# Performance work log

Measured on AMD Instinct MI355X. Metric: run time of the kernel, lower is better.

The kernel has to match this reference:

```python
import jax, jax.numpy as jnp
import numpy as np

B, S, D, H = 2, 2048, 1024, 16
HD = D // H  # 64


def setup_inputs() -> dict:
    key = jax.random.key(0)
    ks = jax.random.split(key, 10)
    sc = 1.0 / np.sqrt(D)
    return {
        "decoder_hs": jax.random.normal(ks[0], (B, S, D), jnp.float32),
        "encoder_hs": jax.random.normal(ks[1], (B, S, D), jnp.float32),
        "Wq": jax.random.normal(ks[2], (D, D), jnp.float32) * sc,
        "bq": jax.random.normal(ks[3], (D,), jnp.float32) * 0.02,
        "Wk": jax.random.normal(ks[4], (D, D), jnp.float32) * sc,
        "bk": jax.random.normal(ks[5], (D,), jnp.float32) * 0.02,
        "Wv": jax.random.normal(ks[6], (D, D), jnp.float32) * sc,
        "bv": jax.random.normal(ks[7], (D,), jnp.float32) * 0.02,
        "Wp": jax.random.normal(ks[8], (D, D), jnp.float32) * sc,
        "bp": jax.random.normal(ks[9], (D,), jnp.float32) * 0.02,
    }


def reference(decoder_hs, encoder_hs, Wq, bq, Wk, bk, Wv, bv, Wp, bp):
    b, s, d = decoder_hs.shape
    # torch nn.Linear: y = x @ W.T + b, W is [out, in]
    q = decoder_hs @ Wq.T + bq
    k = encoder_hs @ Wk.T + bk
    v = encoder_hs @ Wv.T + bv
    # head split: [b, s, d] -> [b, h, s, hd]
    q = q.reshape(b, s, H, HD).transpose(0, 2, 1, 3)
    k = k.reshape(b, s, H, HD).transpose(0, 2, 1, 3)
    v = v.reshape(b, s, H, HD).transpose(0, 2, 1, 3)
    scale = 1.0 / np.sqrt(HD).astype(np.float32)
    att = jnp.einsum('bhqd,bhkd->bhqk', q, k) * scale
    att = jax.nn.softmax(att, axis=-1)
    y = jnp.einsum('bhqk,bhkd->bhqd', att, v)
    y = y.transpose(0, 2, 1, 3).reshape(b, s, d)
    return y @ Wp.T + bp
```

## Files before the change

kernel.cpp:

```cpp
#include <hip/hip_runtime.h>
#include <hip/hip_bf16.h>
#include <cstdint>
#include <cstddef>

#define BB 2
#define SS 2048
#define DD 1024
#define HH 16
#define HD 64

typedef __attribute__((ext_vector_type(8))) short bf16x8;
typedef __attribute__((ext_vector_type(4))) float f32x4;
typedef __attribute__((ext_vector_type(16))) float f32x16;

#define GLL(g, l) __builtin_amdgcn_global_load_lds( \
    (const __attribute__((address_space(1))) void*)(g), \
    (__attribute__((address_space(3))) void*)(l), 16, 0, 0)

__device__ __forceinline__ short f2bf_fast(float f) {
    uint32_t u = __float_as_uint(f);
    u += 0x7FFF + ((u >> 16) & 1);
    return (short)(u >> 16);
}
__device__ __forceinline__ uint32_t pack_bf2(float a, float b) {
    uint32_t ua = __float_as_uint(a), ub = __float_as_uint(b);
    ua += 0x7FFF + ((ua >> 16) & 1);
    ub += 0x7FFF + ((ub >> 16) & 1);
    return (ua >> 16) | (ub & 0xFFFF0000u);
}
__device__ __forceinline__ uint32_t cvtpk_bf2(float a, float b) {
    uint32_t r;
    asm("v_cvt_pk_bf16_f32 %0, %1, %2" : "=v"(r) : "v"(a), "v"(b));
    return r;
}
__device__ __forceinline__ void pl32swap(uint32_t& a, uint32_t& b) {
    asm("v_permlane32_swap_b32 %0, %1" : "+v"(a), "+v"(b));
}
__device__ __forceinline__ bf16x8 cvt8(const float* __restrict__ p) {
    float4 a = *(const float4*)p;
    float4 b = *(const float4*)(p + 4);
    union { uint32_t d[4]; bf16x8 v; } r;
    r.d[0] = pack_bf2(a.x, a.y);
    r.d[1] = pack_bf2(a.z, a.w);
    r.d[2] = pack_bf2(b.x, b.y);
    r.d[3] = pack_bf2(b.z, b.w);
    return r.v;
}

__global__ __launch_bounds__(256) void cvt6_kernel(
    const float* __restrict__ s0, const float* __restrict__ s1,
    const float* __restrict__ s2, const float* __restrict__ s3,
    const float* __restrict__ s4, const float* __restrict__ s5,
    short* __restrict__ d0, short* __restrict__ d1, short* __restrict__ d2,
    short* __restrict__ d3, short* __restrict__ d4, short* __restrict__ d5)
{
    const int id = blockIdx.x * 256 + threadIdx.x;
    const float* s; short* d; size_t off;
    if (id < 1048576) {
        int e = id >> 19;
        off = (size_t)(id & 524287) * 8;
        s = e ? s1 : s0;  d = e ? d1 : d0;
    } else {
        int j = id - 1048576;
        int w = j >> 17;
        off = (size_t)(j & 131071) * 8;
        s = (w == 0) ? s2 : (w == 1) ? s3 : (w == 2) ? s4 : s5;
        d = (w == 0) ? d2 : (w == 1) ? d3 : (w == 2) ? d4 : d5;
    }
    bf16x8 r = cvt8(s + off);
    *(uint4*)(d + off) = *(uint4*)&r;
}

template<int BF>
__global__ __launch_bounds__(256, 3) void qkv_gemm_kernel(
    const void* __restrict__ dec, const void* __restrict__ enc,
    const void* __restrict__ Wq, const void* __restrict__ Wk,
    const void* __restrict__ Wv,
    const float* __restrict__ bq, const float* __restrict__ bk,
    const float* __restrict__ bv,
    short* __restrict__ Qo, short* __restrict__ Ko, short* __restrict__ Vo)
{
    __shared__ short As[128 * 64];
    __shared__ short Bs[128 * 64];

    const int z = blockIdx.z;
    const void* Xv = (z == 0) ? dec : enc;
    const void* Wp_ = (z == 0) ? Wq : (z == 1) ? Wk : Wv;
    const float* bias = (z == 0) ? bq : (z == 1) ? bk : bv;
    short* Yo = (z == 0) ? Qo : (z == 1) ? Ko : Vo;
    const float qs = (z == 0) ? (0.125f * 1.44269504088896f) : 1.0f;

    const int t = threadIdx.x;
    const int lane = t & 63, wv = t >> 6;
    const int lr = lane & 15, quad = lane >> 4;
    const int e7 = lr & 7;
    const int wm = wv >> 1, wn = wv & 1;
    const int m0 = blockIdx.y * 128;
    const int n0 = blockIdx.x * 128;
    const int K = DD;

    f32x4 acc[4][4];
    #pragma unroll
    for (int i = 0; i < 4; i++)
        #pragma unroll
        for (int j = 0; j < 4; j++) acc[i][j] = (f32x4){0.f, 0.f, 0.f, 0.f};

    for (int kb = 0; kb < K; kb += 64) {
        __syncthreads();
        if (BF) {
            const short* Xb = (const short*)Xv;
            const short* Wb = (const short*)Wp_;
            #pragma unroll
            for (int c = 0; c < 4; c++) {
                int r0 = wv * 32 + c * 8;
                int r = r0 + (lane >> 3);
                int sc = ((lane & 7) ^ (r & 7)) * 8;
                GLL(Xb + (size_t)(m0 + r) * K + kb + sc, &As[r0 * 64]);
                GLL(Wb + (size_t)(n0 + r) * K + kb + sc, &Bs[r0 * 64]);
            }
        } else {
            const float* Xf = (const float*)Xv;
            const float* Wf = (const float*)Wp_;
            #pragma unroll
            for (int c = 0; c < 4; c++) {
                int id = t + c * 256;
                int r = id >> 3, lc = id & 7;
                int pc = (lc ^ (r & 7)) * 8;
                *(bf16x8*)&As[r * 64 + pc] = cvt8(Xf + (size_t)(m0 + r) * K + kb + lc * 8);
                *(bf16x8*)&Bs[r * 64 + pc] = cvt8(Wf + (size_t)(n0 + r) * K + kb + lc * 8);
            }
        }
        __syncthreads();

        bf16x8 af[4][2], bfr[4][2];
        #pragma unroll
        for (int kk = 0; kk < 2; kk++) {
            int pc = ((kk * 4 + quad) ^ e7) * 8;
            #pragma unroll
            for (int mi = 0; mi < 4; mi++)
                af[mi][kk] = *(const bf16x8*)&As[(wm * 64 + mi * 16 + lr) * 64 + pc];
            #pragma unroll
            for (int ni = 0; ni < 4; ni++)
                bfr[ni][kk] = *(const bf16x8*)&Bs[(wn * 64 + ni * 16 + lr) * 64 + pc];
        }
        #pragma unroll
        for (int kk = 0; kk < 2; kk++)
            #pragma unroll
            for (int mi = 0; mi < 4; mi++)
                #pragma unroll
                for (int ni = 0; ni < 4; ni++)
                    acc[mi][ni] = __builtin_amdgcn_mfma_f32_16x16x32_bf16(
                        af[mi][kk], bfr[ni][kk], acc[mi][ni], 0, 0, 0);
    }

    if (z < 2) {
        #pragma unroll
        for (int ni = 0; ni < 4; ni++) {
            int col = n0 + wn * 64 + ni * 16 + lr;
            int h = col >> 6, hd = col & 63;
            float bvv = bias[col];
            #pragma unroll
            for (int mi = 0; mi < 4; mi++) {
                #pragma unroll
                for (int r2 = 0; r2 < 4; r2++) {
                    int row = m0 + wm * 64 + mi * 16 + quad * 4 + r2;
                    int b = row >> 11, s = row & 2047;
                    float v = (acc[mi][ni][r2] + bvv) * qs;
                    size_t off = ((size_t)(b * HH + h) * SS + s) * HD + hd;
                    Yo[off] = f2bf_fast(v);
                }
            }
        }
    } else {
        #pragma unroll
        for (int ni = 0; ni < 4; ni++) {
            int col = n0 + wn * 64 + ni * 16 + lr;
            int h = col >> 6, hd = col & 63;
            float bvv = bias[col];
            #pragma unroll
            for (int mi = 0; mi < 4; mi++) {
                int s0 = m0 + wm * 64 + mi * 16 + quad * 4;
                int b = s0 >> 11, s = s0 & 2047;
                union { uint32_t d[2]; } u;
                u.d[0] = pack_bf2(acc[mi][ni][0] + bvv, acc[mi][ni][1] + bvv);
                u.d[1] = pack_bf2(acc[mi][ni][2] + bvv, acc[mi][ni][3] + bvv);
                size_t off = ((size_t)(b * HH + h) * HD + hd) * SS + s;
                *(uint2*)(Yo + off) = *(uint2*)&u;
            }
        }
    }
}

template<int WBF>
__global__ __launch_bounds__(256, 2) void proj_gemm_kernel(
    const short* __restrict__ X,
    const void* __restrict__ W, const float* __restrict__ bias,
    float* __restrict__ Y)
{
    __shared__ short As[64 * 32];
    __shared__ short Bs[128 * 32];

    const int t = threadIdx.x;
    const int lane = t & 63, wv = t >> 6;
    const int lr = lane & 15, quad = lane >> 4;
    const int wm = wv >> 1, wn = wv & 1;
    const int m0 = blockIdx.y * 64;
    const int n0 = blockIdx.x * 128;
    const int K = DD, N = DD;

    f32x4 acc[2][4];
    #pragma unroll
    for (int i = 0; i < 2; i++)
        #pragma unroll
        for (int j = 0; j < 4; j++) acc[i][j] = (f32x4){0.f, 0.f, 0.f, 0.f};

    for (int kb = 0; kb < K; kb += 32) {
        __syncthreads();
        {
            int r0 = wv * 16;
            int r = r0 + (lane >> 2), ch = (lane & 3) * 8;
            GLL(X + (size_t)(m0 + r) * K + kb + ch, &As[r0 * 32]);
        }
        if (WBF) {
            const short* Wb = (const short*)W;
            #pragma unroll
            for (int c = 0; c < 2; c++) {
                int r0 = wv * 32 + c * 16;
                int r = r0 + (lane >> 2), ch = (lane & 3) * 8;
                GLL(Wb + (size_t)(n0 + r) * K + kb + ch, &Bs[r0 * 32]);
            }
        } else {
            const float* Wf = (const float*)W;
            #pragma unroll
            for (int c = 0; c < 2; c++) {
                int id = t + c * 256;
                int r = id >> 2, c8 = (id & 3) * 8;
                *(bf16x8*)&Bs[r * 32 + c8] = cvt8(Wf + (size_t)(n0 + r) * K + kb + c8);
            }
        }
        __syncthreads();

        bf16x8 af[2], bfr[4];
        #pragma unroll
        for (int mi = 0; mi < 2; mi++)
            af[mi] = *(const bf16x8*)&As[(wm * 32 + mi * 16 + lr) * 32 + quad * 8];
        #pragma unroll
        for (int ni = 0; ni < 4; ni++)
            bfr[ni] = *(const bf16x8*)&Bs[(wn * 64 + ni * 16 + lr) * 32 + quad * 8];
        #pragma unroll
        for (int mi = 0; mi < 2; mi++)
            #pragma unroll
            for (int ni = 0; ni < 4; ni++)
                acc[mi][ni] = __builtin_amdgcn_mfma_f32_16x16x32_bf16(
                    af[mi], bfr[ni], acc[mi][ni], 0, 0, 0);
    }

    #pragma unroll
    for (int ni = 0; ni < 4; ni++) {
        int col = n0 + wn * 64 + ni * 16 + lr;
        float bvv = bias[col];
        #pragma unroll
        for (int mi = 0; mi < 2; mi++) {
            #pragma unroll
            for (int r2 = 0; r2 < 4; r2++) {
                int row = m0 + wm * 32 + mi * 16 + quad * 4 + r2;
                Y[(size_t)row * N + col] = acc[mi][ni][r2] + bvv;
            }
        }
    }
}

__global__ __launch_bounds__(256, 2) void attn_kernel(
    const short* __restrict__ Q,
    const short* __restrict__ Kgl,
    const short* __restrict__ Vt_g,
    short* __restrict__ Y)
{
    __shared__ short Ks[2][128][64];
    __shared__ short Vt[2][64][128];

    const int t = threadIdx.x;
    const int lane = t & 63, w = t >> 6;
    const int lq = lane & 31, hf = lane >> 5;
    const int gl = (lq & 7) ^ ((lq >> 3) & 3);

    const int bid = blockIdx.x;
    const int slot = bid >> 3;
    const int bh = ((slot >> 4) << 3) + (bid & 7);
    const int qt = slot & 15;
    const int b = bh >> 4, h = bh & 15;

    const int q = qt * 128 + w * 32 + lq;
    const short* Qp = Q + ((size_t)bh * SS + q) * HD;
    bf16x8 qf[4];
    #pragma unroll
    for (int j = 0; j < 4; j++)
        qf[j] = *(const bf16x8*)(Qp + j * 16 + hf * 8);

    f32x16 o[2];
    #pragma unroll
    for (int i = 0; i < 16; i++) { o[0][i] = 0.f; o[1][i] = 0.f; }
    f32x4 vsum = (f32x4){0.f, 0.f, 0.f, 0.f};

    const short* Kb = Kgl + (size_t)bh * SS * HD;
    const short* Vb = Vt_g + (size_t)bh * HD * SS;

    auto stage = [&](int kt1, int nb) {
        #pragma unroll
        for (int c = 0; c < 4; c++) {
            int r0 = w * 32 + c * 8;
            int r  = r0 + (lane >> 3);
            int g  = (r & 7) ^ ((r >> 3) & 3);
            int sc = ((lane & 7) ^ g) * 8;
            GLL(Kb + (size_t)(kt1 * 128 + r) * 64 + sc, &Ks[nb][r0][0]);
        }
        #pragma unroll
        for (int c = 0; c < 4; c++) {
            int h0 = w * 16 + c * 4;
            int hd = h0 + (lane >> 4);
            int g  = (hd & 7) ^ ((hd >> 3) & 3);
            int s16 = (lane & 15) ^ g;
            GLL(Vb + (size_t)hd * SS + kt1 * 128 + s16 * 8, &Vt[nb][h0][0]);
        }
    };

    stage(0, 0);
    __syncthreads();

    int cur = 0;
    for (int kt = 0; kt < SS / 128; kt++) {
        if (kt + 1 < SS / 128) stage(kt + 1, cur ^ 1);

        bf16x8 pb[4][2];
        #pragma unroll
        for (int s = 0; s < 4; s++) {
            const short* krow = &Ks[cur][s * 32 + lq][0];
            f32x16 sc = (f32x16){0.f,0.f,0.f,0.f,0.f,0.f,0.f,0.f,
                                 0.f,0.f,0.f,0.f,0.f,0.f,0.f,0.f};
            __builtin_amdgcn_s_setprio(1);
            #pragma unroll
            for (int j = 0; j < 4; j++) {
                bf16x8 kf = *(const bf16x8*)&krow[((j * 2 + hf) ^ gl) * 8];
                sc = __builtin_amdgcn_mfma_f32_32x32x16_bf16(kf, qf[j], sc, 0, 0, 0);
            }
            __builtin_amdgcn_s_setprio(0);

            float ev[16];
            #pragma unroll
            for (int i = 0; i < 16; i++) ev[i] = __builtin_amdgcn_exp2f(sc[i]);
            #pragma unroll
            for (int r = 0; r < 4; r++)
                vsum += (f32x4){ev[4*r], ev[4*r+1], ev[4*r+2], ev[4*r+3]};
            uint32_t dw[8];
            #pragma unroll
            for (int i = 0; i < 8; i++) dw[i] = cvtpk_bf2(ev[2*i], ev[2*i+1]);
            pl32swap(dw[0], dw[2]); pl32swap(dw[1], dw[3]);
            pl32swap(dw[4], dw[6]); pl32swap(dw[5], dw[7]);
            union { uint32_t u[4]; bf16x8 v; } f0, f1;
            f0.u[0] = dw[0]; f0.u[1] = dw[1]; f0.u[2] = dw[2]; f0.u[3] = dw[3];
            f1.u[0] = dw[4]; f1.u[1] = dw[5]; f1.u[2] = dw[6]; f1.u[3] = dw[7];
            pb[s][0] = f0.v; pb[s][1] = f1.v;
        }

        __builtin_amdgcn_s_setprio(1);
        #pragma unroll
        for (int ds = 0; ds < 2; ds++) {
            const short* vrow = &Vt[cur][ds * 32 + lq][0];
            #pragma unroll
            for (int s = 0; s < 4; s++)
                #pragma unroll
                for (int c = 0; c < 2; c++) {
                    bf16x8 va = *(const bf16x8*)&vrow[((s * 4 + c * 2 + hf) ^ gl) * 8];
                    o[ds] = __builtin_amdgcn_mfma_f32_32x32x16_bf16(
                        va, pb[s][c], o[ds], 0, 0, 0);
                }
        }
        __builtin_amdgcn_s_setprio(0);

        __syncthreads();
        cur ^= 1;
    }

    float lsum = (vsum[0] + vsum[1]) + (vsum[2] + vsum[3]);
    lsum += __shfl_xor(lsum, 32, 64);
    float inv = 1.0f / lsum;

    short* Yp = Y + ((size_t)b * SS + q) * DD + h * 64 + hf * 4;
    #pragma unroll
    for (int ds = 0; ds < 2; ds++)
        #pragma unroll
        for (int rr = 0; rr < 4; rr++) {
            union { uint32_t d[2]; } u;
            u.d[0] = pack_bf2(o[ds][rr*4+0] * inv, o[ds][rr*4+1] * inv);
            u.d[1] = pack_bf2(o[ds][rr*4+2] * inv, o[ds][rr*4+3] * inv);
            *(uint2*)(Yp + ds * 32 + rr * 8) = *(uint2*)&u;
        }
}

extern "C" void kernel_launch(void* const* d_in, const int* in_sizes, int n_in,
                              void* d_out, int out_size, void* d_ws, size_t ws_size,
                              hipStream_t stream) {
    const float* dec = (const float*)d_in[0];
    const float* enc = (const float*)d_in[1];
    const float* Wq  = (const float*)d_in[2];
    const float* bq  = (const float*)d_in[3];
    const float* Wk  = (const float*)d_in[4];
    const float* bk  = (const float*)d_in[5];
    const float* Wv  = (const float*)d_in[6];
    const float* bv  = (const float*)d_in[7];
    const float* Wp  = (const float*)d_in[8];
    const float* bp  = (const float*)d_in[9];

    const size_t per = (size_t)BB * HH * SS * HD;
    const size_t wsz = (size_t)DD * DD;
    short* ws = (short*)d_ws;
    short* Qb  = ws;
    short* Kb  = ws + per;
    short* Vtb = ws + 2 * per;
    short* Yb  = ws + 3 * per;

    dim3 qkv_grid(DD / 128, (BB * SS) / 128, 3);
    dim3 proj_grid(DD / 128, (BB * SS) / 64);
    const int attn_blocks = BB * HH * (SS / 128);
    const int cvt_blocks = (2 * 524288 + 4 * 131072) / 256;

    const size_t need = (6 * per + 4 * wsz) * sizeof(short);
    if (ws_size >= need) {
        short* decb = ws + 4 * per;
        short* encb = ws + 5 * per;
        short* Wqb  = ws + 6 * per;
        short* Wkb  = Wqb + wsz;
        short* Wvb  = Wqb + 2 * wsz;
        short* Wpb  = Wqb + 3 * wsz;
        cvt6_kernel<<<cvt_blocks, 256, 0, stream>>>(
            dec, enc, Wq, Wk, Wv, Wp, decb, encb, Wqb, Wkb, Wvb, Wpb);
        qkv_gemm_kernel<1><<<qkv_grid, 256, 0, stream>>>(
            decb, encb, Wqb, Wkb, Wvb, bq, bk, bv, Qb, Kb, Vtb);
        attn_kernel<<<attn_blocks, 256, 0, stream>>>(Qb, Kb, Vtb, Yb);
        proj_gemm_kernel<1><<<proj_grid, 256, 0, stream>>>(Yb, Wpb, bp, (float*)d_out);
    } else {
        qkv_gemm_kernel<0><<<qkv_grid, 256, 0, stream>>>(
            dec, enc, Wq, Wk, Wv, bq, bk, bv, Qb, Kb, Vtb);
        attn_kernel<<<attn_blocks, 256, 0, stream>>>(Qb, Kb, Vtb, Yb);
        proj_gemm_kernel<0><<<proj_grid, 256, 0, stream>>>(Yb, Wp, bp, (float*)d_out);
    }
}
```

Before: 195.5 us.

## Double K-tile in projection GEMM with XOR swizzle; interleave QK MFMA chains in attention

The projection GEMM now stages 64-wide K slices instead of 32, which halves the number of barrier-separated iterations. It also adds an XOR swizzle to the LDS layout so the wider rows are read without bank conflicts. In the attention kernel, the four independent QK^T accumulation chains are computed interleaved before any exponentiation, so consecutive MFMAs do not depend on each other. The cost is doubled LDS use in the GEMM and more live accumulator registers in attention, which could lower occupancy.

```diff
diff --git a/kernel.cpp b/kernel.cpp
--- a/kernel.cpp
+++ b/kernel.cpp
@@ -197,12 +197,13 @@
     const void* __restrict__ W, const float* __restrict__ bias,
     float* __restrict__ Y)
 {
-    __shared__ short As[64 * 32];
-    __shared__ short Bs[128 * 32];
+    __shared__ short As[64 * 64];
+    __shared__ short Bs[128 * 64];
 
     const int t = threadIdx.x;
     const int lane = t & 63, wv = t >> 6;
     const int lr = lane & 15, quad = lane >> 4;
+    const int e7 = lr & 7;
     const int wm = wv >> 1, wn = wv & 1;
     const int m0 = blockIdx.y * 64;
     const int n0 = blockIdx.x * 128;
@@ -214,45 +215,57 @@
         #pragma unroll
         for (int j = 0; j < 4; j++) acc[i][j] = (f32x4){0.f, 0.f, 0.f, 0.f};
 
-    for (int kb = 0; kb < K; kb += 32) {
+    for (int kb = 0; kb < K; kb += 64) {
         __syncthreads();
         {
-            int r0 = wv * 16;
-            int r = r0 + (lane >> 2), ch = (lane & 3) * 8;
-            GLL(X + (size_t)(m0 + r) * K + kb + ch, &As[r0 * 32]);
+            #pragma unroll
+            for (int c = 0; c < 2; c++) {
+                int r0 = wv * 16 + c * 8;
+                int r = r0 + (lane >> 3);
+                int sc = ((lane & 7) ^ (r & 7)) * 8;
+                GLL(X + (size_t)(m0 + r) * K + kb + sc, &As[r0 * 64]);
+            }
         }
         if (WBF) {
             const short* Wb = (const short*)W;
             #pragma unroll
-            for (int c = 0; c < 2; c++) {
-                int r0 = wv * 32 + c * 16;
-                int r = r0 + (lane >> 2), ch = (lane & 3) * 8;
-                GLL(Wb + (size_t)(n0 + r) * K + kb + ch, &Bs[r0 * 32]);
+            for (int c = 0; c < 4; c++) {
+                int r0 = wv * 32 + c * 8;
+                int r = r0 + (lane >> 3);
+                int sc = ((lane & 7) ^ (r & 7)) * 8;
+                GLL(Wb + (size_t)(n0 + r) * K + kb + sc, &Bs[r0 * 64]);
             }
         } else {
             const float* Wf = (const float*)W;
             #pragma unroll
-            for (int c = 0; c < 2; c++) {
+            for (int c = 0; c < 4; c++) {
                 int id = t + c * 256;
-                int r = id >> 2, c8 = (id & 3) * 8;
-                *(bf16x8*)&Bs[r * 32 + c8] = cvt8(Wf + (size_t)(n0 + r) * K + kb + c8);
+                int r = id >> 3, lc = id & 7;
+                int pc = (lc ^ (r & 7)) * 8;
+                *(bf16x8*)&Bs[r * 64 + pc] = cvt8(Wf + (size_t)(n0 + r) * K + kb + lc * 8);
             }
         }
         __syncthreads();
 
-        bf16x8 af[2], bfr[4];
-        #pragma unroll
-        for (int mi = 0; mi < 2; mi++)
-            af[mi] = *(const bf16x8*)&As[(wm * 32 + mi * 16 + lr) * 32 + quad * 8];
-        #pragma unroll
-        for (int ni = 0; ni < 4; ni++)
-            bfr[ni] = *(const bf16x8*)&Bs[(wn * 64 + ni * 16 + lr) * 32 + quad * 8];
-        #pragma unroll
-        for (int mi = 0; mi < 2; mi++)
+        bf16x8 af[2][2], bfr[4][2];
+        #pragma unroll
+        for (int kk = 0; kk < 2; kk++) {
+            int pc = ((kk * 4 + quad) ^ e7) * 8;
+            #pragma unroll
+            for (int mi = 0; mi < 2; mi++)
+                af[mi][kk] = *(const bf16x8*)&As[(wm * 32 + mi * 16 + lr) * 64 + pc];
             #pragma unroll
             for (int ni = 0; ni < 4; ni++)
-                acc[mi][ni] = __builtin_amdgcn_mfma_f32_16x16x32_bf16(
-                    af[mi], bfr[ni], acc[mi][ni], 0, 0, 0);
+                bfr[ni][kk] = *(const bf16x8*)&Bs[(wn * 64 + ni * 16 + lr) * 64 + pc];
+        }
+        #pragma unroll
+        for (int kk = 0; kk < 2; kk++)
+            #pragma unroll
+            for (int mi = 0; mi < 2; mi++)
+                #pragma unroll
+                for (int ni = 0; ni < 4; ni++)
+                    acc[mi][ni] = __builtin_amdgcn_mfma_f32_16x16x32_bf16(
+                        af[mi][kk], bfr[ni][kk], acc[mi][ni], 0, 0, 0);
     }
 
     #pragma unroll
@@ -331,23 +344,29 @@
     for (int kt = 0; kt < SS / 128; kt++) {
         if (kt + 1 < SS / 128) stage(kt + 1, cur ^ 1);
 
+        f32x16 sc[4];
+        #pragma unroll
+        for (int s = 0; s < 4; s++)
+            #pragma unroll
+            for (int i = 0; i < 16; i++) sc[s][i] = 0.f;
+        __builtin_amdgcn_s_setprio(1);
+        #pragma unroll
+        for (int j = 0; j < 4; j++)
+            #pragma unroll
+            for (int s = 0; s < 4; s++) {
+                const short* krow = &Ks[cur][s * 32 + lq][0];
+                bf16x8 kf = *(const bf16x8*)&krow[((j * 2 + hf) ^ gl) * 8];
+                sc[s] = __builtin_amdgcn_mfma_f32_32x32x16_bf16(
+                    kf, qf[j], sc[s], 0, 0, 0);
+            }
+        __builtin_amdgcn_s_setprio(0);
+
         bf16x8 pb[4][2];
         #pragma unroll
         for (int s = 0; s < 4; s++) {
-            const short* krow = &Ks[cur][s * 32 + lq][0];
-            f32x16 sc = (f32x16){0.f,0.f,0.f,0.f,0.f,0.f,0.f,0.f,
-                                 0.f,0.f,0.f,0.f,0.f,0.f,0.f,0.f};
-            __builtin_amdgcn_s_setprio(1);
-            #pragma unroll
-            for (int j = 0; j < 4; j++) {
-                bf16x8 kf = *(const bf16x8*)&krow[((j * 2 + hf) ^ gl) * 8];
-                sc = __builtin_amdgcn_mfma_f32_32x32x16_bf16(kf, qf[j], sc, 0, 0, 0);
-            }
-            __builtin_amdgcn_s_setprio(0);
-
             float ev[16];
             #pragma unroll
-            for (int i = 0; i < 16; i++) ev[i] = __builtin_amdgcn_exp2f(sc[i]);
+            for (int i = 0; i < 16; i++) ev[i] = __builtin_amdgcn_exp2f(sc[s][i]);
             #pragma unroll
             for (int r = 0; r < 4; r++)
                 vsum += (f32x4){ev[4*r], ev[4*r+1], ev[4*r+2], ev[4*r+3]};
```

After: 199.1 us. About the same (+1.8%).

## Give each wave private K/V LDS tiles and drop block-wide barriers

Applied to the files above, without the earlier changes.

Each of the four waves now stages its own copy of the K and V^T tiles, 32 keys per step, into a private LDS region. Block-wide __syncthreads are replaced with per-wave waitcnt and sched_barrier. The aim is to remove cross-wave barrier stalls so waves can drift independently. In exchange every wave loads the full K/V stream itself, quadrupling global/L2 traffic per block. The shorter key tile also doubles loop iterations and leaves less MFMA work per iteration to hide load latency.

```diff
diff --git a/kernel.cpp b/kernel.cpp
--- a/kernel.cpp
+++ b/kernel.cpp
@@ -276,13 +276,13 @@
     const short* __restrict__ Vt_g,
     short* __restrict__ Y)
 {
-    __shared__ short Ks[2][128][64];
-    __shared__ short Vt[2][64][128];
+    __shared__ short smem[32768];
 
     const int t = threadIdx.x;
     const int lane = t & 63, w = t >> 6;
     const int lq = lane & 31, hf = lane >> 5;
     const int gl = (lq & 7) ^ ((lq >> 3) & 3);
+    const int vl = lq & 3;
 
     const int bid = blockIdx.x;
     const int slot = bid >> 3;
@@ -305,79 +305,76 @@
     const short* Kb = Kgl + (size_t)bh * SS * HD;
     const short* Vb = Vt_g + (size_t)bh * HD * SS;
 
+    short* wbase = smem + w * 8192;
+
     auto stage = [&](int kt1, int nb) {
+        short* Kd = wbase + nb * 2048;
+        short* Vd = wbase + 4096 + nb * 2048;
         #pragma unroll
         for (int c = 0; c < 4; c++) {
-            int r0 = w * 32 + c * 8;
-            int r  = r0 + (lane >> 3);
-            int g  = (r & 7) ^ ((r >> 3) & 3);
+            int r = c * 8 + (lane >> 3);
+            int g = (r & 7) ^ ((r >> 3) & 3);
             int sc = ((lane & 7) ^ g) * 8;
-            GLL(Kb + (size_t)(kt1 * 128 + r) * 64 + sc, &Ks[nb][r0][0]);
+            GLL(Kb + (size_t)(kt1 * 32 + r) * HD + sc, Kd + c * 8 * 64);
         }
         #pragma unroll
         for (int c = 0; c < 4; c++) {
-            int h0 = w * 16 + c * 4;
-            int hd = h0 + (lane >> 4);
-            int g  = (hd & 7) ^ ((hd >> 3) & 3);
-            int s16 = (lane & 15) ^ g;
-            GLL(Vb + (size_t)hd * SS + kt1 * 128 + s16 * 8, &Vt[nb][h0][0]);
+            int hd = c * 16 + (lane >> 2);
+            int sc = ((lane & 3) ^ (hd & 3)) * 8;
+            GLL(Vb + (size_t)hd * SS + kt1 * 32 + sc, Vd + c * 16 * 32);
         }
     };
 
     stage(0, 0);
-    __syncthreads();
+    asm volatile("s_waitcnt vmcnt(0)" ::: "memory");
+    __builtin_amdgcn_sched_barrier(0);
 
     int cur = 0;
-    for (int kt = 0; kt < SS / 128; kt++) {
-        if (kt + 1 < SS / 128) stage(kt + 1, cur ^ 1);
-
-        bf16x8 pb[4][2];
-        #pragma unroll
-        for (int s = 0; s < 4; s++) {
-            const short* krow = &Ks[cur][s * 32 + lq][0];
-            f32x16 sc = (f32x16){0.f,0.f,0.f,0.f,0.f,0.f,0.f,0.f,
-                                 0.f,0.f,0.f,0.f,0.f,0.f,0.f,0.f};
-            __builtin_amdgcn_s_setprio(1);
-            #pragma unroll
-            for (int j = 0; j < 4; j++) {
-                bf16x8 kf = *(const bf16x8*)&krow[((j * 2 + hf) ^ gl) * 8];
-                sc = __builtin_amdgcn_mfma_f32_32x32x16_bf16(kf, qf[j], sc, 0, 0, 0);
-            }
-            __builtin_amdgcn_s_setprio(0);
-
-            float ev[16];
-            #pragma unroll
-            for (int i = 0; i < 16; i++) ev[i] = __builtin_amdgcn_exp2f(sc[i]);
-            #pragma unroll
-            for (int r = 0; r < 4; r++)
-                vsum += (f32x4){ev[4*r], ev[4*r+1], ev[4*r+2], ev[4*r+3]};
-            uint32_t dw[8];
-            #pragma unroll
-            for (int i = 0; i < 8; i++) dw[i] = cvtpk_bf2(ev[2*i], ev[2*i+1]);
-            pl32swap(dw[0], dw[2]); pl32swap(dw[1], dw[3]);
-            pl32swap(dw[4], dw[6]); pl32swap(dw[5], dw[7]);
-            union { uint32_t u[4]; bf16x8 v; } f0, f1;
-            f0.u[0] = dw[0]; f0.u[1] = dw[1]; f0.u[2] = dw[2]; f0.u[3] = dw[3];
-            f1.u[0] = dw[4]; f1.u[1] = dw[5]; f1.u[2] = dw[6]; f1.u[3] = dw[7];
-            pb[s][0] = f0.v; pb[s][1] = f1.v;
-        }
-
+    for (int kt = 0; kt < SS / 32; kt++) {
+        if (kt + 1 < SS / 32) stage(kt + 1, cur ^ 1);
+
+        const short* Kc = wbase + cur * 2048;
+        const short* Vc = wbase + 4096 + cur * 2048;
+
+        f32x16 sc16 = (f32x16){0.f,0.f,0.f,0.f,0.f,0.f,0.f,0.f,
+                               0.f,0.f,0.f,0.f,0.f,0.f,0.f,0.f};
         __builtin_amdgcn_s_setprio(1);
         #pragma unroll
+        for (int j = 0; j < 4; j++) {
+            bf16x8 kf = *(const bf16x8*)&Kc[lq * 64 + ((j * 2 + hf) ^ gl) * 8];
+            sc16 = __builtin_amdgcn_mfma_f32_32x32x16_bf16(kf, qf[j], sc16, 0, 0, 0);
+        }
+        __builtin_amdgcn_s_setprio(0);
+
+        float ev[16];
+        #pragma unroll
+        for (int i = 0; i < 16; i++) ev[i] = __builtin_amdgcn_exp2f(sc16[i]);
+        #pragma unroll
+        for (int r = 0; r < 4; r++)
+            vsum += (f32x4){ev[4*r], ev[4*r+1], ev[4*r+2], ev[4*r+3]};
+        uint32_t dw[8];
+        #pragma unroll
+        for (int i = 0; i < 8; i++) dw[i] = cvtpk_bf2(ev[2*i], ev[2*i+1]);
+        pl32swap(dw[0], dw[2]); pl32swap(dw[1], dw[3]);
+        pl32swap(dw[4], dw[6]); pl32swap(dw[5], dw[7]);
+        union { uint32_t u[4]; bf16x8 v; } f0, f1;
+        f0.u[0] = dw[0]; f0.u[1] = dw[1]; f0.u[2] = dw[2]; f0.u[3] = dw[3];
+        f1.u[0] = dw[4]; f1.u[1] = dw[5]; f1.u[2] = dw[6]; f1.u[3] = dw[7];
+        bf16x8 pb0 = f0.v, pb1 = f1.v;
+
+        __builtin_amdgcn_s_setprio(1);
+        #pragma unroll
         for (int ds = 0; ds < 2; ds++) {
-            const short* vrow = &Vt[cur][ds * 32 + lq][0];
-            #pragma unroll
-            for (int s = 0; s < 4; s++)
-                #pragma unroll
-                for (int c = 0; c < 2; c++) {
-                    bf16x8 va = *(const bf16x8*)&vrow[((s * 4 + c * 2 + hf) ^ gl) * 8];
-                    o[ds] = __builtin_amdgcn_mfma_f32_32x32x16_bf16(
-                        va, pb[s][c], o[ds], 0, 0, 0);
-                }
+            const short* vrow = &Vc[(ds * 32 + lq) * 32];
+            bf16x8 va0 = *(const bf16x8*)&vrow[((0 + hf) ^ vl) * 8];
+            o[ds] = __builtin_amdgcn_mfma_f32_32x32x16_bf16(va0, pb0, o[ds], 0, 0, 0);
+            bf16x8 va1 = *(const bf16x8*)&vrow[((2 + hf) ^ vl) * 8];
+            o[ds] = __builtin_amdgcn_mfma_f32_32x32x16_bf16(va1, pb1, o[ds], 0, 0, 0);
         }
         __builtin_amdgcn_s_setprio(0);
 
-        __syncthreads();
+        asm volatile("s_waitcnt vmcnt(0) lgkmcnt(0)" ::: "memory");
+        __builtin_amdgcn_sched_barrier(0);
         cur ^= 1;
     }
 
```

After: 207.1 us. +6.0%, slower.

## Software-pipeline attention: overlap PV of previous tile with softmax of current

Applied to the files above, without the earlier changes.

Restructures the attention loop so QK^T for tile kt is issued in one batch, then the PV matmuls for tile kt-1 are interleaved with the exp/convert softmax work of tile kt using sched_group_barrier hints. V is triple-buffered in LDS so the previous tile's V stays resident while the next one streams in. The aim is to hide transcendental and VALU latency behind MFMA work. In exchange it uses more LDS and registers (two P buffers, four score accumulators), which may pressure occupancy at 2 blocks per CU.

```diff
diff --git a/kernel.cpp b/kernel.cpp
--- a/kernel.cpp
+++ b/kernel.cpp
@@ -277,7 +277,7 @@
     short* __restrict__ Y)
 {
     __shared__ short Ks[2][128][64];
-    __shared__ short Vt[2][64][128];
+    __shared__ short Vt[3][64][128];
 
     const int t = threadIdx.x;
     const int lane = t & 63, w = t >> 6;
@@ -305,14 +305,16 @@
     const short* Kb = Kgl + (size_t)bh * SS * HD;
     const short* Vb = Vt_g + (size_t)bh * HD * SS;
 
-    auto stage = [&](int kt1, int nb) {
+    auto stage = [&](int kt1) {
+        short* Kd = &Ks[kt1 & 1][0][0];
+        short* Vd = &Vt[kt1 % 3][0][0];
         #pragma unroll
         for (int c = 0; c < 4; c++) {
             int r0 = w * 32 + c * 8;
             int r  = r0 + (lane >> 3);
             int g  = (r & 7) ^ ((r >> 3) & 3);
             int sc = ((lane & 7) ^ g) * 8;
-            GLL(Kb + (size_t)(kt1 * 128 + r) * 64 + sc, &Ks[nb][r0][0]);
+            GLL(Kb + (size_t)(kt1 * 128 + r) * 64 + sc, Kd + r0 * 64);
         }
         #pragma unroll
         for (int c = 0; c < 4; c++) {
@@ -320,66 +322,104 @@
             int hd = h0 + (lane >> 4);
             int g  = (hd & 7) ^ ((hd >> 3) & 3);
             int s16 = (lane & 15) ^ g;
-            GLL(Vb + (size_t)hd * SS + kt1 * 128 + s16 * 8, &Vt[nb][h0][0]);
+            GLL(Vb + (size_t)hd * SS + kt1 * 128 + s16 * 8, Vd + h0 * 128);
         }
     };
 
-    stage(0, 0);
+    auto qk = [&](int kt, f32x16 (&sc)[4]) {
+        const short (*Kc)[64] = Ks[kt & 1];
+        __builtin_amdgcn_s_setprio(1);
+        #pragma unroll
+        for (int j = 0; j < 4; j++)
+            #pragma unroll
+            for (int s = 0; s < 4; s++) {
+                bf16x8 kf = *(const bf16x8*)&Kc[s * 32 + lq][((j * 2 + hf) ^ gl) * 8];
+                sc[s] = __builtin_amdgcn_mfma_f32_32x32x16_bf16(kf, qf[j], sc[s], 0, 0, 0);
+            }
+        __builtin_amdgcn_s_setprio(0);
+    };
+
+    auto sm = [&](const f32x16& scs, bf16x8& p0, bf16x8& p1) {
+        float ev[16];
+        #pragma unroll
+        for (int i = 0; i < 16; i++) ev[i] = __builtin_amdgcn_exp2f(scs[i]);
+        #pragma unroll
+        for (int r = 0; r < 4; r++)
+            vsum += (f32x4){ev[4*r], ev[4*r+1], ev[4*r+2], ev[4*r+3]};
+        uint32_t dw[8];
+        #pragma unroll
+        for (int i = 0; i < 8; i++) dw[i] = cvtpk_bf2(ev[2*i], ev[2*i+1]);
+        pl32swap(dw[0], dw[2]); pl32swap(dw[1], dw[3]);
+        pl32swap(dw[4], dw[6]); pl32swap(dw[5], dw[7]);
+        union { uint32_t u[4]; bf16x8 v; } f0, f1;
+        f0.u[0] = dw[0]; f0.u[1] = dw[1]; f0.u[2] = dw[2]; f0.u[3] = dw[3];
+        f1.u[0] = dw[4]; f1.u[1] = dw[5]; f1.u[2] = dw[6]; f1.u[3] = dw[7];
+        p0 = f0.v; p1 = f1.v;
+    };
+
+    auto pv4 = [&](const short* Vc, int s, bf16x8 p0, bf16x8 p1) {
+        #pragma unroll
+        for (int ds = 0; ds < 2; ds++) {
+            const short* vrow = Vc + (ds * 32 + lq) * 128;
+            bf16x8 va0 = *(const bf16x8*)&vrow[((s * 4 + 0 + hf) ^ gl) * 8];
+            o[ds] = __builtin_amdgcn_mfma_f32_32x32x16_bf16(va0, p0, o[ds], 0, 0, 0);
+            bf16x8 va1 = *(const bf16x8*)&vrow[((s * 4 + 2 + hf) ^ gl) * 8];
+            o[ds] = __builtin_amdgcn_mfma_f32_32x32x16_bf16(va1, p1, o[ds], 0, 0, 0);
+        }
+    };
+
+    bf16x8 pbA[4][2], pbB[4][2];
+
+    auto body = [&](int kt, bf16x8 (&pbp)[4][2], bf16x8 (&pbc)[4][2]) {
+        if (kt + 1 < 16) stage(kt + 1);
+        f32x16 sc[4];
+        #pragma unroll
+        for (int s = 0; s < 4; s++)
+            #pragma unroll
+            for (int i = 0; i < 16; i++) sc[s][i] = 0.f;
+        qk(kt, sc);
+        __builtin_amdgcn_sched_barrier(0);
+        const short* Vprev = &Vt[(kt + 2) % 3][0][0];
+        __builtin_amdgcn_s_setprio(1);
+        #pragma unroll
+        for (int s = 0; s < 4; s++) {
+            pv4(Vprev, s, pbp[s][0], pbp[s][1]);
+            sm(sc[s], pbc[s][0], pbc[s][1]);
+            __builtin_amdgcn_sched_group_barrier(0x100, 4, 0);
+            __builtin_amdgcn_sched_group_barrier(0x008, 4, 0);
+            __builtin_amdgcn_sched_group_barrier(0x001, 32, 0);
+        }
+        __builtin_amdgcn_s_setprio(0);
+        __syncthreads();
+    };
+
+    stage(0);
     __syncthreads();
 
-    int cur = 0;
-    for (int kt = 0; kt < SS / 128; kt++) {
-        if (kt + 1 < SS / 128) stage(kt + 1, cur ^ 1);
-
-        bf16x8 pb[4][2];
-        #pragma unroll
-        for (int s = 0; s < 4; s++) {
-            const short* krow = &Ks[cur][s * 32 + lq][0];
-            f32x16 sc = (f32x16){0.f,0.f,0.f,0.f,0.f,0.f,0.f,0.f,
-                                 0.f,0.f,0.f,0.f,0.f,0.f,0.f,0.f};
-            __builtin_amdgcn_s_setprio(1);
-            #pragma unroll
-            for (int j = 0; j < 4; j++) {
-                bf16x8 kf = *(const bf16x8*)&krow[((j * 2 + hf) ^ gl) * 8];
-                sc = __builtin_amdgcn_mfma_f32_32x32x16_bf16(kf, qf[j], sc, 0, 0, 0);
-            }
-            __builtin_amdgcn_s_setprio(0);
-
-            float ev[16];
-            #pragma unroll
-            for (int i = 0; i < 16; i++) ev[i] = __builtin_amdgcn_exp2f(sc[i]);
-            #pragma unroll
-            for (int r = 0; r < 4; r++)
-                vsum += (f32x4){ev[4*r], ev[4*r+1], ev[4*r+2], ev[4*r+3]};
-            uint32_t dw[8];
-            #pragma unroll
-            for (int i = 0; i < 8; i++) dw[i] = cvtpk_bf2(ev[2*i], ev[2*i+1]);
-            pl32swap(dw[0], dw[2]); pl32swap(dw[1], dw[3]);
-            pl32swap(dw[4], dw[6]); pl32swap(dw[5], dw[7]);
-            union { uint32_t u[4]; bf16x8 v; } f0, f1;
-            f0.u[0] = dw[0]; f0.u[1] = dw[1]; f0.u[2] = dw[2]; f0.u[3] = dw[3];
-            f1.u[0] = dw[4]; f1.u[1] = dw[5]; f1.u[2] = dw[6]; f1.u[3] = dw[7];
-            pb[s][0] = f0.v; pb[s][1] = f1.v;
-        }
-
-        __builtin_amdgcn_s_setprio(1);
-        #pragma unroll
-        for (int ds = 0; ds < 2; ds++) {
-            const short* vrow = &Vt[cur][ds * 32 + lq][0];
-            #pragma unroll
-            for (int s = 0; s < 4; s++)
-                #pragma unroll
-                for (int c = 0; c < 2; c++) {
-                    bf16x8 va = *(const bf16x8*)&vrow[((s * 4 + c * 2 + hf) ^ gl) * 8];
-                    o[ds] = __builtin_amdgcn_mfma_f32_32x32x16_bf16(
-                        va, pb[s][c], o[ds], 0, 0, 0);
-                }
-        }
-        __builtin_amdgcn_s_setprio(0);
-
-        __syncthreads();
-        cur ^= 1;
-    }
+    {
+        stage(1);
+        f32x16 sc[4];
+        #pragma unroll
+        for (int s = 0; s < 4; s++)
+            #pragma unroll
+            for (int i = 0; i < 16; i++) sc[s][i] = 0.f;
+        qk(0, sc);
+        __builtin_amdgcn_sched_barrier(0);
+        #pragma unroll
+        for (int s = 0; s < 4; s++) sm(sc[s], pbA[s][0], pbA[s][1]);
+        __syncthreads();
+    }
+
+    for (int kt = 1; kt <= 13; kt += 2) {
+        body(kt, pbA, pbB);
+        body(kt + 1, pbB, pbA);
+    }
+    body(15, pbA, pbB);
+
+    __builtin_amdgcn_s_setprio(1);
+    #pragma unroll
+    for (int s = 0; s < 4; s++) pv4(&Vt[0][0][0], s, pbB[s][0], pbB[s][1]);
+    __builtin_amdgcn_s_setprio(0);
 
     float lsum = (vsum[0] + vsum[1]) + (vsum[2] + vsum[3]);
     lsum += __shfl_xor(lsum, 32, 64);
```

Measured after the change: 194.6 us. About the same (-0.5%).
